# Kernel tuning notes

Hardware: AMD Instinct MI355X
Metric: run time of the kernel (lower is better)

Reference implementation:

```python
import jax, jax.numpy as jnp
import numpy as np

HIDDEN = 2048
KEY = 2048
EPS = 1e-05


def setup_inputs() -> dict:
    key = jax.random.key(0)
    k1, k2, k3 = jax.random.split(key, 3)
    B, S = 4, 2048
    x = jax.random.normal(k1, (B, S, HIDDEN), dtype=jnp.float32)
    # kaiming_uniform_ bound for fan_in=HIDDEN (a=sqrt(5) default): sqrt(6/((1+5)*fan_in)) = 1/sqrt(fan_in)
    bq = 1.0 / np.sqrt(HIDDEN)
    qkv = jax.random.uniform(k2, (HIDDEN, KEY * 3), minval=-bq, maxval=bq, dtype=jnp.float32)
    bo = 1.0 / np.sqrt(KEY)
    o_proj = jax.random.uniform(k3, (KEY, HIDDEN), minval=-bo, maxval=bo, dtype=jnp.float32)
    gamma = jnp.ones((HIDDEN,), dtype=jnp.float32)
    beta = jnp.zeros((HIDDEN,), dtype=jnp.float32)
    return {"x": x, "qkv": qkv, "o_proj": o_proj, "gamma": gamma, "beta": beta}


def reference(x, qkv, o_proj, gamma, beta):
    residual = x
    # LayerNorm over last dim
    mu = jnp.mean(x, axis=-1, keepdims=True)
    var = jnp.mean((x - mu) ** 2, axis=-1, keepdims=True)
    x_norm = (x - mu) / jnp.sqrt(var + EPS) * gamma + beta
    q = x_norm @ qkv[:, :KEY]          # [B,S,K]
    k = x_norm @ qkv[:, KEY:2 * KEY]   # [B,S,K]
    v = x_norm @ qkv[:, 2 * KEY:]      # [B,S,K]
    scale = 1.0 / jnp.sqrt(jnp.float32(KEY))
    scores = jnp.einsum('bsk,btk->bst', q, k) * scale  # [B,S,S]
    S_len = x.shape[1]
    causal = jnp.tril(jnp.ones((S_len, S_len), dtype=bool))
    scores = jnp.where(causal[None], scores, -jnp.inf)
    attn = jax.nn.softmax(scores, axis=-1)
    out = attn @ v          # [B,S,K]
    out = out @ o_proj      # [B,S,H]
    return out + residual
```

## Files before the change

### kernel.cpp

```cpp
#include <hip/hip_runtime.h>
#include <stdint.h>

typedef short short8 __attribute__((ext_vector_type(8)));
typedef unsigned short ushort8 __attribute__((ext_vector_type(8)));
typedef unsigned short ushort4v __attribute__((ext_vector_type(4)));
typedef float f32x4 __attribute__((ext_vector_type(4)));

#define HD 2048
#define S_LEN 2048
#define NROWS 8192
#define N3 6144

typedef __attribute__((address_space(3))) void lds_void_t;
typedef __attribute__((address_space(1))) void g_void_t;

__device__ inline void gload_lds16(const void* g, void* l) {
    __builtin_amdgcn_global_load_lds((g_void_t*)g, (lds_void_t*)l, 16, 0, 0);
}

__device__ inline unsigned short f2bf(float f) {
    unsigned u = __float_as_uint(f);
    unsigned r = (u + 0x7FFFu + ((u >> 16) & 1u)) >> 16;
    return (unsigned short)r;
}
__device__ inline float bf2f(unsigned short h) {
    return __uint_as_float(((unsigned)h) << 16);
}

__global__ __launch_bounds__(256) void ln_kernel(const float* __restrict__ x,
    const float* __restrict__ gamma, const float* __restrict__ beta,
    unsigned short* __restrict__ xn) {
    int row = blockIdx.x;
    const float* xr = x + (size_t)row * HD;
    int tid = threadIdx.x;
    float v[8];
    float4 a = *(const float4*)(xr + tid * 8);
    float4 b = *(const float4*)(xr + tid * 8 + 4);
    v[0]=a.x; v[1]=a.y; v[2]=a.z; v[3]=a.w; v[4]=b.x; v[5]=b.y; v[6]=b.z; v[7]=b.w;
    float s = 0.f, ss = 0.f;
#pragma unroll
    for (int e = 0; e < 8; e++) { s += v[e]; ss += v[e] * v[e]; }
    for (int off = 32; off > 0; off >>= 1) {
        s += __shfl_down(s, off);
        ss += __shfl_down(ss, off);
    }
    __shared__ float red[10];
    int wave = tid >> 6, lane = tid & 63;
    if (lane == 0) { red[wave] = s; red[4 + wave] = ss; }
    __syncthreads();
    if (tid == 0) {
        float S = red[0] + red[1] + red[2] + red[3];
        float SS = red[4] + red[5] + red[6] + red[7];
        float mu = S * (1.0f / HD);
        float var = SS * (1.0f / HD) - mu * mu;
        red[8] = mu;
        red[9] = rsqrtf(var + 1e-5f);
    }
    __syncthreads();
    float mu = red[8], rstd = red[9];
#pragma unroll
    for (int e = 0; e < 8; e++) {
        int c = tid * 8 + e;
        float val = (v[e] - mu) * rstd * gamma[c] + beta[c];
        xn[(size_t)row * HD + c] = f2bf(val);
    }
}

__global__ __launch_bounds__(256) void transp_f32_bf16(const float* __restrict__ src, int ld_s,
    unsigned short* __restrict__ dst, int ld_d) {
    __shared__ float tile[32][33];
    int c0 = blockIdx.x * 32, r0 = blockIdx.y * 32;
    int tc = threadIdx.x & 31, tr = threadIdx.x >> 5;
#pragma unroll
    for (int i = 0; i < 32; i += 8)
        tile[tr + i][tc] = src[(size_t)(r0 + tr + i) * ld_s + c0 + tc];
    __syncthreads();
#pragma unroll
    for (int i = 0; i < 32; i += 8)
        dst[(size_t)(c0 + tr + i) * ld_d + r0 + tc] = f2bf(tile[tc][tr + i]);
}

__global__ __launch_bounds__(256) void softmax_causal(unsigned short* __restrict__ sc) {
    int r = blockIdx.x;
    int s = r & (S_LEN - 1);
    unsigned short* row = sc + (size_t)r * S_LEN;
    int tid = threadIdx.x;
    ushort8 u = *(const ushort8*)(row + tid * 8);
    float v[8];
    float mx = -3.0e38f;
#pragma unroll
    for (int e = 0; e < 8; e++) {
        int t = tid * 8 + e;
        float f = bf2f(u[e]);
        v[e] = (t <= s) ? f : -3.0e38f;
        mx = fmaxf(mx, v[e]);
    }
    for (int off = 32; off > 0; off >>= 1) mx = fmaxf(mx, __shfl_down(mx, off));
    __shared__ float red[8];
    int wave = tid >> 6, lane = tid & 63;
    if (lane == 0) red[wave] = mx;
    __syncthreads();
    mx = fmaxf(fmaxf(red[0], red[1]), fmaxf(red[2], red[3]));
    float ex[8];
    float sum = 0.f;
#pragma unroll
    for (int e = 0; e < 8; e++) {
        ex[e] = (v[e] > -1.0e38f) ? __expf(v[e] - mx) : 0.f;
        sum += ex[e];
    }
    for (int off = 32; off > 0; off >>= 1) sum += __shfl_down(sum, off);
    if (lane == 0) red[4 + wave] = sum;
    __syncthreads();
    float inv = 1.0f / (red[4] + red[5] + red[6] + red[7]);
#pragma unroll
    for (int e = 0; e < 8; e++) {
        row[tid * 8 + e] = f2bf(ex[e] * inv);
    }
}

template <int EPI>
__global__ __launch_bounds__(256) void gemm_nt(
    const unsigned short* __restrict__ Ab, int lda, long sAz,
    const unsigned short* __restrict__ Bb, int ldb, long sBz,
    void* __restrict__ Cb, int ldc, long sCz,
    int kdim, int causal, float scale, const float* __restrict__ resid,
    unsigned short* __restrict__ vt) {
    int bx = blockIdx.x, by = blockIdx.y, bz = blockIdx.z;
    if (causal) by = gridDim.y - 1 - by;
    if (causal == 1 && bx > by) return;
    const unsigned short* A = Ab + (size_t)bz * sAz;
    const unsigned short* Bt = Bb + (size_t)bz * sBz;
    int kmax = kdim;
    if (causal == 2) { int km = (by + 1) * 128; if (km < kmax) kmax = km; }
    int m0 = by * 128, n0 = bx * 128;

    __shared__ unsigned short lA[128 * 64];
    __shared__ unsigned short lB[128 * 64];

    int tid = threadIdx.x;
    int wave = tid >> 6, lane = tid & 63;
    int quad = lane >> 4, l16 = lane & 15;
    int wr = wave >> 1, wc = wave & 1;

    int rstage = wave * 32 + (lane >> 2);
    int ck = (lane & 3) * 8;
    const unsigned short* gA[2][2];
    const unsigned short* gB[2][2];
    unsigned short* ldA[2][2];
    unsigned short* ldB[2][2];
#pragma unroll
    for (int r16 = 0; r16 < 2; r16++)
#pragma unroll
        for (int h = 0; h < 2; h++) {
            gA[r16][h] = A + (size_t)(m0 + rstage + r16 * 16) * lda + h * 32 + ck;
            gB[r16][h] = Bt + (size_t)(n0 + rstage + r16 * 16) * ldb + h * 32 + ck;
            ldA[r16][h] = &lA[h * 4096 + (wave * 32 + r16 * 16) * 32];
            ldB[r16][h] = &lB[h * 4096 + (wave * 32 + r16 * 16) * 32];
        }

    f32x4 acc[4][4] = {};

    for (int k0 = 0; k0 < kmax; k0 += 64) {
        __syncthreads();
#pragma unroll
        for (int r16 = 0; r16 < 2; r16++)
#pragma unroll
            for (int h = 0; h < 2; h++) {
                gload_lds16(gA[r16][h], ldA[r16][h]);
                gload_lds16(gB[r16][h], ldB[r16][h]);
            }
        __syncthreads();
#pragma unroll
        for (int h = 0; h < 2; h++) {
            short8 af[4], bfr[4];
#pragma unroll
            for (int i = 0; i < 4; i++)
                af[i] = *(const short8*)&lA[h * 4096 + (wr * 64 + i * 16 + l16) * 32 + quad * 8];
#pragma unroll
            for (int j = 0; j < 4; j++)
                bfr[j] = *(const short8*)&lB[h * 4096 + (wc * 64 + j * 16 + l16) * 32 + quad * 8];
#pragma unroll
            for (int i = 0; i < 4; i++)
#pragma unroll
                for (int j = 0; j < 4; j++)
                    acc[i][j] = __builtin_amdgcn_mfma_f32_16x16x32_bf16(af[i], bfr[j], acc[i][j], 0, 0, 0);
        }
#pragma unroll
        for (int r16 = 0; r16 < 2; r16++)
#pragma unroll
            for (int h = 0; h < 2; h++) { gA[r16][h] += 64; gB[r16][h] += 64; }
    }

    int row0 = m0 + wr * 64 + quad * 4;
    int col0 = n0 + wc * 64 + l16;
    if (EPI == 3 && n0 >= 4096) {
        int batch = m0 >> 11;
        int sl0 = (m0 & 2047) + wr * 64 + quad * 4;
#pragma unroll
        for (int j = 0; j < 4; j++) {
            int kcol = (n0 - 4096) + wc * 64 + j * 16 + l16;
            unsigned short* base = vt + (size_t)batch * S_LEN * S_LEN + (size_t)kcol * S_LEN + sl0;
#pragma unroll
            for (int i = 0; i < 4; i++) {
                ushort4v p;
#pragma unroll
                for (int r = 0; r < 4; r++) p[r] = f2bf(acc[i][j][r]);
                *(ushort4v*)(base + i * 16) = p;
            }
        }
    } else if (EPI == 0 || EPI == 1 || EPI == 3) {
        unsigned short* C = (unsigned short*)Cb + (size_t)bz * sCz;
#pragma unroll
        for (int i = 0; i < 4; i++)
#pragma unroll
            for (int r = 0; r < 4; r++) {
                int row = row0 + i * 16 + r;
#pragma unroll
                for (int j = 0; j < 4; j++) {
                    float v = acc[i][j][r];
                    if (EPI == 1) v *= scale;
                    C[(size_t)row * ldc + col0 + j * 16] = f2bf(v);
                }
            }
    } else {
        float* C = (float*)Cb + (size_t)bz * sCz;
#pragma unroll
        for (int i = 0; i < 4; i++)
#pragma unroll
            for (int r = 0; r < 4; r++) {
                int row = row0 + i * 16 + r;
#pragma unroll
                for (int j = 0; j < 4; j++) {
                    int col = col0 + j * 16;
                    C[(size_t)row * ldc + col] = acc[i][j][r] + resid[(size_t)row * ldc + col];
                }
            }
    }
}

extern "C" void kernel_launch(void* const* d_in, const int* in_sizes, int n_in,
                              void* d_out, int out_size, void* d_ws, size_t ws_size,
                              hipStream_t stream) {
    const float* x      = (const float*)d_in[0];
    const float* qkv    = (const float*)d_in[1];
    const float* o_proj = (const float*)d_in[2];
    const float* gamma  = (const float*)d_in[3];
    const float* beta   = (const float*)d_in[4];
    float* out = (float*)d_out;

    char* w = (char*)d_ws;
    unsigned short* xn      = (unsigned short*)(w);
    unsigned short* w_t     = (unsigned short*)(w + 33554432);
    unsigned short* o_t     = (unsigned short*)(w + 58720256);
    unsigned short* qkv_out = (unsigned short*)(w + 67108864);
    unsigned short* v_t     = (unsigned short*)(w + 167772160);
    unsigned short* scores  = xn;

    ln_kernel<<<NROWS, 256, 0, stream>>>(x, gamma, beta, xn);
    transp_f32_bf16<<<dim3(192, 64), 256, 0, stream>>>(qkv, N3, w_t, HD);
    transp_f32_bf16<<<dim3(64, 64), 256, 0, stream>>>(o_proj, HD, o_t, HD);
    gemm_nt<3><<<dim3(48, 64, 1), 256, 0, stream>>>(xn, HD, 0L, w_t, HD, 0L,
        (void*)qkv_out, N3, 0L, HD, 0, 1.0f, nullptr, v_t);
    float scale = 0.022097086912079608f;
    gemm_nt<1><<<dim3(16, 16, 4), 256, 0, stream>>>(qkv_out, N3, (long)S_LEN * N3,
        qkv_out + 2048, N3, (long)S_LEN * N3,
        (void*)scores, S_LEN, (long)S_LEN * S_LEN, HD, 1, scale, nullptr, nullptr);
    softmax_causal<<<NROWS, 256, 0, stream>>>(scores);
    gemm_nt<0><<<dim3(16, 16, 4), 256, 0, stream>>>(scores, S_LEN, (long)S_LEN * S_LEN,
        v_t, S_LEN, (long)HD * S_LEN,
        (void*)qkv_out, N3, (long)S_LEN * N3, S_LEN, 2, 1.0f, nullptr, nullptr);
    gemm_nt<2><<<dim3(16, 64, 1), 256, 0, stream>>>(qkv_out, N3, 0L, o_t, HD, 0L,
        (void*)out, HD, 0L, HD, 0, 1.0f, x, nullptr);
}
```

Before: 660.4 us.

## Split-K the attention GEMMs into two halves and merge in softmax and a pass

Splits the QK^T and PV GEMMs into two K-chunks of 1024, doubling the grid so more blocks run on the causal triangle. The two partial scores are summed in bf16 inside a modified softmax, and the two PV partials are summed by a new merge kernel. The two weight transposes are merged into one launch. The cost is extra memory traffic for the partial buffers, an extra kernel, and bf16 rounding of the partials before they are summed.

```diff
diff --git a/kernel.cpp b/kernel.cpp
--- a/kernel.cpp
+++ b/kernel.cpp
@@ -66,10 +66,14 @@
     }
 }
 
-__global__ __launch_bounds__(256) void transp_f32_bf16(const float* __restrict__ src, int ld_s,
-    unsigned short* __restrict__ dst, int ld_d) {
+__global__ __launch_bounds__(256) void transp_weights(const float* __restrict__ qkv,
+    unsigned short* __restrict__ w_t, const float* __restrict__ o_proj,
+    unsigned short* __restrict__ o_t) {
     __shared__ float tile[32][33];
-    int c0 = blockIdx.x * 32, r0 = blockIdx.y * 32;
+    const float* src; unsigned short* dst; int ld_s, ld_d, bx;
+    if (blockIdx.x < 192) { src = qkv; dst = w_t; ld_s = N3; ld_d = HD; bx = blockIdx.x; }
+    else { src = o_proj; dst = o_t; ld_s = HD; ld_d = HD; bx = blockIdx.x - 192; }
+    int c0 = bx * 32, r0 = blockIdx.y * 32;
     int tc = threadIdx.x & 31, tr = threadIdx.x >> 5;
 #pragma unroll
     for (int i = 0; i < 32; i += 8)
@@ -80,18 +84,21 @@
         dst[(size_t)(c0 + tr + i) * ld_d + r0 + tc] = f2bf(tile[tc][tr + i]);
 }
 
-__global__ __launch_bounds__(256) void softmax_causal(unsigned short* __restrict__ sc) {
+__global__ __launch_bounds__(256) void softmax_causal2(unsigned short* __restrict__ sc0,
+    const unsigned short* __restrict__ sc1) {
     int r = blockIdx.x;
     int s = r & (S_LEN - 1);
-    unsigned short* row = sc + (size_t)r * S_LEN;
+    unsigned short* row0 = sc0 + (size_t)r * S_LEN;
+    const unsigned short* row1 = sc1 + (size_t)r * S_LEN;
     int tid = threadIdx.x;
-    ushort8 u = *(const ushort8*)(row + tid * 8);
+    ushort8 u0 = *(const ushort8*)(row0 + tid * 8);
+    ushort8 u1 = *(const ushort8*)(row1 + tid * 8);
     float v[8];
     float mx = -3.0e38f;
 #pragma unroll
     for (int e = 0; e < 8; e++) {
         int t = tid * 8 + e;
-        float f = bf2f(u[e]);
+        float f = bf2f(u0[e]) + bf2f(u1[e]);
         v[e] = (t <= s) ? f : -3.0e38f;
         mx = fmaxf(mx, v[e]);
     }
@@ -114,8 +121,25 @@
     float inv = 1.0f / (red[4] + red[5] + red[6] + red[7]);
 #pragma unroll
     for (int e = 0; e < 8; e++) {
-        row[tid * 8 + e] = f2bf(ex[e] * inv);
-    }
+        row0[tid * 8 + e] = f2bf(ex[e] * inv);
+    }
+}
+
+__global__ __launch_bounds__(256) void merge_pv(const unsigned short* __restrict__ pv0,
+    const unsigned short* __restrict__ pv1, unsigned short* __restrict__ attn) {
+    int r = blockIdx.x;
+    int s = r & (S_LEN - 1);
+    int tid = threadIdx.x;
+    const ushort8 a = *(const ushort8*)(pv0 + (size_t)r * HD + tid * 8);
+    ushort8 o;
+    if (s >= 1024) {
+        const ushort8 b = *(const ushort8*)(pv1 + (size_t)r * HD + tid * 8);
+#pragma unroll
+        for (int e = 0; e < 8; e++) o[e] = f2bf(bf2f(a[e]) + bf2f(b[e]));
+    } else {
+        o = a;
+    }
+    *(ushort8*)(attn + (size_t)r * HD + tid * 8) = o;
 }
 
 template <int EPI>
@@ -123,15 +147,22 @@
     const unsigned short* __restrict__ Ab, int lda, long sAz,
     const unsigned short* __restrict__ Bb, int ldb, long sBz,
     void* __restrict__ Cb, int ldc, long sCz,
-    int kdim, int causal, float scale, const float* __restrict__ resid,
+    int kdim, int causal, int kchunk, long cKofs,
+    float scale, const float* __restrict__ resid,
     unsigned short* __restrict__ vt) {
-    int bx = blockIdx.x, by = blockIdx.y, bz = blockIdx.z;
+    constexpr int KSPLIT = (EPI == 0 || EPI == 1) ? 2 : 1;
+    int bx = blockIdx.x, by = blockIdx.y;
+    int bz = blockIdx.z, kc = 0;
+    if (KSPLIT == 2) { bz = blockIdx.z >> 1; kc = blockIdx.z & 1; }
     if (causal) by = gridDim.y - 1 - by;
     if (causal == 1 && bx > by) return;
+    int kfull = kdim;
+    if (causal == 2) { int km = (by + 1) * 128; if (km < kfull) kfull = km; }
+    int koff = kc * kchunk;
+    int kend = koff + kchunk; if (kend > kfull) kend = kfull;
+    if (kend <= koff) return;
     const unsigned short* A = Ab + (size_t)bz * sAz;
     const unsigned short* Bt = Bb + (size_t)bz * sBz;
-    int kmax = kdim;
-    if (causal == 2) { int km = (by + 1) * 128; if (km < kmax) kmax = km; }
     int m0 = by * 128, n0 = bx * 128;
 
     __shared__ unsigned short lA[128 * 64];
@@ -142,30 +173,31 @@
     int quad = lane >> 4, l16 = lane & 15;
     int wr = wave >> 1, wc = wave & 1;
 
-    int rstage = wave * 32 + (lane >> 2);
+    int rlane = lane >> 2;
     int ck = (lane & 3) * 8;
     const unsigned short* gA[2][2];
     const unsigned short* gB[2][2];
     unsigned short* ldA[2][2];
     unsigned short* ldB[2][2];
 #pragma unroll
-    for (int r16 = 0; r16 < 2; r16++)
-#pragma unroll
-        for (int h = 0; h < 2; h++) {
-            gA[r16][h] = A + (size_t)(m0 + rstage + r16 * 16) * lda + h * 32 + ck;
-            gB[r16][h] = Bt + (size_t)(n0 + rstage + r16 * 16) * ldb + h * 32 + ck;
-            ldA[r16][h] = &lA[h * 4096 + (wave * 32 + r16 * 16) * 32];
-            ldB[r16][h] = &lB[h * 4096 + (wave * 32 + r16 * 16) * 32];
+    for (int h = 0; h < 2; h++)
+#pragma unroll
+        for (int r16 = 0; r16 < 2; r16++) {
+            int prow = wave * 32 + r16 * 16;
+            gA[r16][h] = A + (size_t)(m0 + prow + rlane) * lda + koff + h * 32 + ck;
+            gB[r16][h] = Bt + (size_t)(n0 + prow + rlane) * ldb + koff + h * 32 + ck;
+            ldA[r16][h] = &lA[h * 4096 + prow * 32];
+            ldB[r16][h] = &lB[h * 4096 + prow * 32];
         }
 
     f32x4 acc[4][4] = {};
 
-    for (int k0 = 0; k0 < kmax; k0 += 64) {
+    for (int k0 = koff; k0 < kend; k0 += 64) {
         __syncthreads();
 #pragma unroll
-        for (int r16 = 0; r16 < 2; r16++)
-#pragma unroll
-            for (int h = 0; h < 2; h++) {
+        for (int h = 0; h < 2; h++)
+#pragma unroll
+            for (int r16 = 0; r16 < 2; r16++) {
                 gload_lds16(gA[r16][h], ldA[r16][h]);
                 gload_lds16(gB[r16][h], ldB[r16][h]);
             }
@@ -186,9 +218,9 @@
                     acc[i][j] = __builtin_amdgcn_mfma_f32_16x16x32_bf16(af[i], bfr[j], acc[i][j], 0, 0, 0);
         }
 #pragma unroll
-        for (int r16 = 0; r16 < 2; r16++)
-#pragma unroll
-            for (int h = 0; h < 2; h++) { gA[r16][h] += 64; gB[r16][h] += 64; }
+        for (int h = 0; h < 2; h++)
+#pragma unroll
+            for (int r16 = 0; r16 < 2; r16++) { gA[r16][h] += 64; gB[r16][h] += 64; }
     }
 
     int row0 = m0 + wr * 64 + quad * 4;
@@ -208,8 +240,8 @@
                 *(ushort4v*)(base + i * 16) = p;
             }
         }
-    } else if (EPI == 0 || EPI == 1 || EPI == 3) {
-        unsigned short* C = (unsigned short*)Cb + (size_t)bz * sCz;
+    } else if (EPI != 2) {
+        unsigned short* C = (unsigned short*)Cb + (size_t)bz * sCz + (size_t)kc * cKofs;
 #pragma unroll
         for (int i = 0; i < 4; i++)
 #pragma unroll
@@ -252,23 +284,29 @@
     unsigned short* xn      = (unsigned short*)(w);
     unsigned short* w_t     = (unsigned short*)(w + 33554432);
     unsigned short* o_t     = (unsigned short*)(w + 58720256);
-    unsigned short* qkv_out = (unsigned short*)(w + 67108864);
-    unsigned short* v_t     = (unsigned short*)(w + 167772160);
-    unsigned short* scores  = xn;
+    unsigned short* qkv2    = (unsigned short*)(w + 67108864);
+    unsigned short* pv0     = (unsigned short*)(w + 67108864);
+    unsigned short* pv1     = (unsigned short*)(w + 100663296);
+    unsigned short* v_t     = (unsigned short*)(w + 134217728);
+    unsigned short* scores0 = xn;
+    unsigned short* scores1 = (unsigned short*)(w + 167772160);
+    unsigned short* attn    = xn;
 
     ln_kernel<<<NROWS, 256, 0, stream>>>(x, gamma, beta, xn);
-    transp_f32_bf16<<<dim3(192, 64), 256, 0, stream>>>(qkv, N3, w_t, HD);
-    transp_f32_bf16<<<dim3(64, 64), 256, 0, stream>>>(o_proj, HD, o_t, HD);
+    transp_weights<<<dim3(256, 64), 256, 0, stream>>>(qkv, w_t, o_proj, o_t);
     gemm_nt<3><<<dim3(48, 64, 1), 256, 0, stream>>>(xn, HD, 0L, w_t, HD, 0L,
-        (void*)qkv_out, N3, 0L, HD, 0, 1.0f, nullptr, v_t);
+        (void*)qkv2, 4096, 0L, HD, 0, HD, 0L, 1.0f, nullptr, v_t);
     float scale = 0.022097086912079608f;
-    gemm_nt<1><<<dim3(16, 16, 4), 256, 0, stream>>>(qkv_out, N3, (long)S_LEN * N3,
-        qkv_out + 2048, N3, (long)S_LEN * N3,
-        (void*)scores, S_LEN, (long)S_LEN * S_LEN, HD, 1, scale, nullptr, nullptr);
-    softmax_causal<<<NROWS, 256, 0, stream>>>(scores);
-    gemm_nt<0><<<dim3(16, 16, 4), 256, 0, stream>>>(scores, S_LEN, (long)S_LEN * S_LEN,
-        v_t, S_LEN, (long)HD * S_LEN,
-        (void*)qkv_out, N3, (long)S_LEN * N3, S_LEN, 2, 1.0f, nullptr, nullptr);
-    gemm_nt<2><<<dim3(16, 64, 1), 256, 0, stream>>>(qkv_out, N3, 0L, o_t, HD, 0L,
-        (void*)out, HD, 0L, HD, 0, 1.0f, x, nullptr);
-}
+    gemm_nt<1><<<dim3(16, 16, 8), 256, 0, stream>>>(qkv2, 4096, (long)S_LEN * 4096,
+        qkv2 + 2048, 4096, (long)S_LEN * 4096,
+        (void*)scores0, S_LEN, (long)S_LEN * S_LEN, HD, 1, 1024,
+        (long)(scores1 - scores0), scale, nullptr, nullptr);
+    softmax_causal2<<<NROWS, 256, 0, stream>>>(scores0, scores1);
+    gemm_nt<0><<<dim3(16, 16, 8), 256, 0, stream>>>(scores0, S_LEN, (long)S_LEN * S_LEN,
+        v_t, S_LEN, (long)S_LEN * S_LEN,
+        (void*)pv0, HD, (long)S_LEN * HD, S_LEN, 2, 1024,
+        (long)(pv1 - pv0), 1.0f, nullptr, nullptr);
+    merge_pv<<<NROWS, 256, 0, stream>>>(pv0, pv1, attn);
+    gemm_nt<2><<<dim3(16, 64, 1), 256, 0, stream>>>(attn, HD, 0L, o_t, HD, 0L,
+        (void*)out, HD, 0L, HD, 0, HD, 0L, 1.0f, x, nullptr);
+}
```

Result: slower. 719.5 us (+8.9%).
